# Kernel tuning notes

Hardware: AMD Instinct MI355X
Metric: run time of the kernel (lower is better)

## Reference

```python
import jax, jax.numpy as jnp
import numpy as np

D_MODEL = 1024
HEADS = 16
D_K = D_MODEL // HEADS  # 64


def setup_inputs() -> dict:
    key = jax.random.key(0)
    ks = jax.random.split(key, 9)
    B, S = 4, 2048
    values = jax.random.normal(ks[0], (B, S, D_MODEL), dtype=jnp.float32)
    keys = jax.random.normal(ks[1], (B, S, D_MODEL), dtype=jnp.float32)
    query = jax.random.normal(ks[2], (B, S, D_MODEL), dtype=jnp.float32)
    mask = jax.random.randint(ks[3], (1, 1, S, S), 0, 2, dtype=jnp.int32)
    # per-head projection weights (shared across heads), torch Linear layout (out, in)
    sc = 1.0 / np.sqrt(D_K)
    Wv = jax.random.uniform(ks[4], (D_K, D_K), jnp.float32, -sc, sc)
    Wk = jax.random.uniform(ks[5], (D_K, D_K), jnp.float32, -sc, sc)
    Wq = jax.random.uniform(ks[6], (D_K, D_K), jnp.float32, -sc, sc)
    so = 1.0 / np.sqrt(D_MODEL)
    Wo = jax.random.uniform(ks[7], (D_MODEL, D_MODEL), jnp.float32, -so, so)
    bo = jax.random.uniform(ks[8], (D_MODEL,), jnp.float32, -so, so)
    return {"values": values, "keys": keys, "query": query, "mask": mask,
            "Wv": Wv, "Wk": Wk, "Wq": Wq, "Wo": Wo, "bo": bo}


def reference(values, keys, query, mask, Wv, Wk, Wq, Wo, bo):
    n, q_len, d = query.shape
    v_len, k_len = values.shape[1], keys.shape[1]
    # reshape to (n, len, heads, d_k) and apply shared per-head linear (x @ W^T)
    v = values.reshape(n, v_len, HEADS, D_K) @ Wv.T
    k = keys.reshape(n, k_len, HEADS, D_K) @ Wk.T
    q = query.reshape(n, q_len, HEADS, D_K) @ Wq.T
    # scores: (n, h, q, k)
    scores = jnp.einsum('nqhd,nkhd->nhqk', q, k)
    scores = jnp.where(mask == 0, jnp.float32(-1e20), scores)
    attn = jax.nn.softmax(scores / jnp.sqrt(jnp.float32(D_K)), axis=3)
    out = jnp.einsum('nhqk,nkhd->nqhd', attn, v).reshape(n, q_len, HEADS * D_K)
    return out @ Wo.T + bo
```

## Files before the change

kernel.cpp:

```cpp
#include <hip/hip_runtime.h>

#define B 4
#define S 2048
#define H 16
#define DK 64
#define DM 1024
#define NTILES (S / 64)
#define QSCALE 0.18033688011112042f

typedef __attribute__((ext_vector_type(8))) short    short8v;
typedef __attribute__((ext_vector_type(4))) short    short4v;
typedef __attribute__((ext_vector_type(4))) float    float4v;
typedef __attribute__((ext_vector_type(4))) unsigned uint4v;

__device__ __forceinline__ unsigned short f2bf(float f) {
    unsigned u = __float_as_uint(f);
    u += 0x7fffu + ((u >> 16) & 1u);
    return (unsigned short)(u >> 16);
}
__device__ __forceinline__ float bf2f(unsigned short h) {
    return __uint_as_float(((unsigned)h) << 16);
}
__device__ __forceinline__ unsigned pk2_rtz(float lo, float hi) {
    return __builtin_amdgcn_perm(__float_as_uint(hi), __float_as_uint(lo), 0x07060302u);
}
__device__ __forceinline__ float fast_exp2(float x) {
#if __has_builtin(__builtin_amdgcn_exp2f)
    return __builtin_amdgcn_exp2f(x);
#else
    return __expf(x * 0.69314718055994531f);
#endif
}
__device__ __forceinline__ short8v cvt8(float4 a, float4 b) {
    short8v r;
    r[0] = (short)f2bf(a.x); r[1] = (short)f2bf(a.y);
    r[2] = (short)f2bf(a.z); r[3] = (short)f2bf(a.w);
    r[4] = (short)f2bf(b.x); r[5] = (short)f2bf(b.y);
    r[6] = (short)f2bf(b.z); r[7] = (short)f2bf(b.w);
    return r;
}
__device__ __forceinline__ void gl2lds16(const void* g, void* l) {
    __builtin_amdgcn_global_load_lds(
        (const __attribute__((address_space(1))) unsigned int*)g,
        (__attribute__((address_space(3))) unsigned int*)l, 16, 0, 0);
}

__global__ __launch_bounds__(256) void mask_pack_kernel(
    const int* __restrict__ mask, unsigned long long* __restrict__ mp)
{
    int t = blockIdx.x * 256 + threadIdx.x;
    int m = mask[t];
    unsigned long long b = __ballot(m != 0);
    if ((threadIdx.x & 63) == 0) mp[t >> 6] = b;
}

__global__ __launch_bounds__(256) void wsplit_kernel(
    const float* __restrict__ Wo, unsigned short* __restrict__ Wh,
    unsigned short* __restrict__ Wl)
{
    int t = (blockIdx.x * 256 + threadIdx.x) * 4;
    float4 wv = *(const float4*)(Wo + t);
    float ws4[4] = {wv.x, wv.y, wv.z, wv.w};
    short4v hv, lv;
    #pragma unroll
    for (int i = 0; i < 4; ++i) {
        unsigned short hi = f2bf(ws4[i]);
        hv[i] = (short)hi;
        lv[i] = (short)f2bf(ws4[i] - bf2f(hi));
    }
    *(short4v*)(Wh + t) = hv;
    *(short4v*)(Wl + t) = lv;
}

__global__ __launch_bounds__(256) void qkv_proj_kernel(
    const float* __restrict__ xv, const float* __restrict__ xk, const float* __restrict__ xq,
    const float* __restrict__ Wv, const float* __restrict__ Wk, const float* __restrict__ Wq,
    unsigned short* __restrict__ vtw, unsigned short* __restrict__ kw, unsigned short* __restrict__ qw)
{
    const int y = blockIdx.y;
    const float* x; const float* W;
    if (y == 0)      { x = xv; W = Wv; }
    else if (y == 1) { x = xk; W = Wk; }
    else             { x = xq; W = Wq; }

    const int tid = threadIdx.x;
    const int w = tid >> 6, L = tid & 63, a = L & 15, g = L >> 4;
    const int bx  = blockIdx.x;
    const int st  = bx & 31;
    const int bh  = bx >> 5;
    const int b_  = bh >> 4, h = bh & 15;
    const int s0b = st * 64;

    short8v wF[4][2];
    #pragma unroll
    for (int t = 0; t < 4; ++t)
        #pragma unroll
        for (int c = 0; c < 2; ++c) {
            const float* wr = W + (size_t)(16 * t + a) * 64 + 32 * c + 8 * g;
            wF[t][c] = cvt8(*(const float4*)wr, *(const float4*)(wr + 4));
        }

    const float* xr = x + ((size_t)(b_ * S) + s0b + 16 * w + a) * DM + h * 64 + 8 * g;
    short8v xF0 = cvt8(*(const float4*)(xr),      *(const float4*)(xr + 4));
    short8v xF1 = cvt8(*(const float4*)(xr + 32), *(const float4*)(xr + 36));

    const float4v z4 = {0.0f, 0.0f, 0.0f, 0.0f};

    if (y == 0) {
        const int c   = 16 * w + a;
        const int pos = 32 * (c >> 5) + 8 * ((c >> 2) & 3) + 4 * ((c >> 4) & 1) + (c & 3);
        #pragma unroll
        for (int mt = 0; mt < 4; ++mt) {
            float4v D = __builtin_amdgcn_mfma_f32_16x16x32_bf16(wF[mt][0], xF0, z4, 0, 0, 0);
            D = __builtin_amdgcn_mfma_f32_16x16x32_bf16(wF[mt][1], xF1, D, 0, 0, 0);
            #pragma unroll
            for (int r = 0; r < 4; ++r)
                vtw[((size_t)bh * 64 + 16 * mt + 4 * g + r) * S + s0b + pos] = f2bf(D[r]);
        }
    } else {
        unsigned short* out = (y == 1) ? kw : qw;
        const float scale = (y == 2) ? QSCALE : 1.0f;
        #pragma unroll
        for (int nt = 0; nt < 4; ++nt) {
            float4v D = __builtin_amdgcn_mfma_f32_16x16x32_bf16(xF0, wF[nt][0], z4, 0, 0, 0);
            D = __builtin_amdgcn_mfma_f32_16x16x32_bf16(xF1, wF[nt][1], D, 0, 0, 0);
            #pragma unroll
            for (int r = 0; r < 4; ++r)
                out[((size_t)bh * S + s0b + 16 * w + 4 * g + r) * 64 + 16 * nt + a] =
                    f2bf(D[r] * scale);
        }
    }
}

__global__ __launch_bounds__(256, 4) void flash_attn_kernel(
    const unsigned short* __restrict__ q, const unsigned short* __restrict__ k,
    const unsigned short* __restrict__ vt, const unsigned long long* __restrict__ mp,
    unsigned short* __restrict__ outh, unsigned short* __restrict__ outl)
{
    __shared__ unsigned short KV[2][2][64 * 64];

    const int tid = threadIdx.x;
    const int w   = tid >> 6;
    const int L   = tid & 63;
    const int a   = L & 15;
    const int g   = L >> 4;
    const int bh  = blockIdx.x;
    const int b_  = bh >> 4, h = bh & 15;
    const int qs  = blockIdx.y * 128 + w * 32;

    const unsigned short* qb = q  + (size_t)bh * S * 64;
    const unsigned short* kb = k  + (size_t)bh * S * 64;
    const unsigned short* vb = vt + (size_t)bh * 64 * S;

    short8v qB[2][2];
    #pragma unroll
    for (int gq = 0; gq < 2; ++gq) {
        const unsigned short* qr = qb + (size_t)(qs + 16 * gq + a) * 64;
        qB[gq][0] = *(const short8v*)(qr +      g * 8);
        qB[gq][1] = *(const short8v*)(qr + 32 + g * 8);
    }

    const unsigned long long* mr0 = mp + (size_t)(qs      + a) * NTILES;
    const unsigned long long* mr1 = mp + (size_t)(qs + 16 + a) * NTILES;

    int srow[2], schk[2];
    #pragma unroll
    for (int i = 0; i < 2; ++i) {
        int p   = (w * 2 + i) * 64 + L;
        srow[i] = p >> 3;
        schk[i] = (p & 7) ^ (srow[i] & 7);
    }

    short8v ones;
    #pragma unroll
    for (int i = 0; i < 8; ++i) ones[i] = (short)0x3F80;

    const float4v z4 = {0.0f, 0.0f, 0.0f, 0.0f};
    float4v o[2][4] = {{z4, z4, z4, z4}, {z4, z4, z4, z4}};
    float4v lD[2] = {z4, z4};

    #pragma unroll
    for (int i = 0; i < 2; ++i) {
        gl2lds16(kb + (size_t)srow[i] * 64 + schk[i] * 8, &KV[0][0][(w * 2 + i) * 64 * 8]);
        gl2lds16(vb + (size_t)srow[i] * S + schk[i] * 8,  &KV[0][1][(w * 2 + i) * 64 * 8]);
    }

    for (int kt = 0; kt < NTILES; ++kt) {
        const int cur = kt & 1;
        __syncthreads();

        if (kt + 1 < NTILES) {
            const int nk = kt + 1;
            #pragma unroll
            for (int i = 0; i < 2; ++i) {
                gl2lds16(kb + ((size_t)(nk * 64 + srow[i])) * 64 + schk[i] * 8,
                         &KV[cur ^ 1][0][(w * 2 + i) * 64 * 8]);
                gl2lds16(vb + (size_t)srow[i] * S + nk * 64 + schk[i] * 8,
                         &KV[cur ^ 1][1][(w * 2 + i) * 64 * 8]);
            }
        }

        const unsigned long long mw0 = mr0[kt];
        const unsigned long long mw1 = mr1[kt];

        const unsigned short* Kb = &KV[cur][0][0];
        const unsigned short* Vb = &KV[cur][1][0];

        short8v kB[4][2], vA[4][2];
        #pragma unroll
        for (int nt = 0; nt < 4; ++nt)
            #pragma unroll
            for (int c = 0; c < 2; ++c) {
                const int off = ((16 * nt + a) * 8 + ((4 * c + g) ^ (a & 7))) * 8;
                kB[nt][c] = *(const short8v*)(Kb + off);
                vA[nt][c] = *(const short8v*)(Vb + off);
            }

        #pragma unroll
        for (int gq = 0; gq < 2; ++gq) {
            float4v st[4];
            #pragma unroll
            for (int nt = 0; nt < 4; ++nt) {
                st[nt] = __builtin_amdgcn_mfma_f32_16x16x32_bf16(kB[nt][0], qB[gq][0], z4, 0, 0, 0);
                st[nt] = __builtin_amdgcn_mfma_f32_16x16x32_bf16(kB[nt][1], qB[gq][1], st[nt], 0, 0, 0);
            }

            const unsigned long long mw = gq ? mw1 : mw0;
            float e[4][4];
            #pragma unroll
            for (int nt = 0; nt < 4; ++nt) {
                unsigned bnt = (unsigned)(mw >> (16 * nt + 4 * g));
                #pragma unroll
                for (int r = 0; r < 4; ++r) {
                    float ee = fast_exp2(st[nt][r]);
                    e[nt][r] = ((bnt >> r) & 1u) ? ee : 0.0f;
                }
            }

            short8v pB[2];
            #pragma unroll
            for (int c = 0; c < 2; ++c) {
                uint4v pu;
                pu[0] = pk2_rtz(e[2*c  ][0], e[2*c  ][1]);
                pu[1] = pk2_rtz(e[2*c  ][2], e[2*c  ][3]);
                pu[2] = pk2_rtz(e[2*c+1][0], e[2*c+1][1]);
                pu[3] = pk2_rtz(e[2*c+1][2], e[2*c+1][3]);
                union { uint4v u; short8v s; } cvt;
                cvt.u = pu;
                pB[c] = cvt.s;
            }

            #pragma unroll
            for (int nt = 0; nt < 4; ++nt) {
                o[gq][nt] = __builtin_amdgcn_mfma_f32_16x16x32_bf16(vA[nt][0], pB[0], o[gq][nt], 0, 0, 0);
                o[gq][nt] = __builtin_amdgcn_mfma_f32_16x16x32_bf16(vA[nt][1], pB[1], o[gq][nt], 0, 0, 0);
            }
            lD[gq] = __builtin_amdgcn_mfma_f32_16x16x32_bf16(ones, pB[0], lD[gq], 0, 0, 0);
            lD[gq] = __builtin_amdgcn_mfma_f32_16x16x32_bf16(ones, pB[1], lD[gq], 0, 0, 0);
        }
    }

    #pragma unroll
    for (int gq = 0; gq < 2; ++gq) {
        const float inv = 1.0f / lD[gq][0];
        const size_t row = (size_t)(b_ * S + qs + 16 * gq + a);
        #pragma unroll
        for (int nt = 0; nt < 4; ++nt) {
            short4v hv, lv;
            #pragma unroll
            for (int r = 0; r < 4; ++r) {
                float v = o[gq][nt][r] * inv;
                unsigned short hi = f2bf(v);
                hv[r] = (short)hi;
                lv[r] = (short)f2bf(v - bf2f(hi));
            }
            const size_t off = row * DM + h * 64 + 16 * nt + 4 * g;
            *(short4v*)(outh + off) = hv;
            *(short4v*)(outl + off) = lv;
        }
    }
}

__global__ __launch_bounds__(256, 2) void out_proj_kernel(
    const unsigned short* __restrict__ Xh, const unsigned short* __restrict__ Xl,
    const unsigned short* __restrict__ Wh, const unsigned short* __restrict__ Wl,
    const float* __restrict__ bo, float* __restrict__ out)
{
    __shared__ unsigned short SAh[128 * 64], SAl[128 * 64];
    __shared__ unsigned short SBh[128 * 64], SBl[128 * 64];

    const int tid = threadIdx.x;
    const int w = tid >> 6, L = tid & 63, a = L & 15, g = L >> 4;
    const int wm = w >> 1, wn = w & 1;
    const int r0 = blockIdx.x * 128;
    const int n0 = blockIdx.y * 128;

    int prow[4], pchk[4], pbase[4];
    #pragma unroll
    for (int i = 0; i < 4; ++i) {
        int p    = w * 256 + i * 64 + L;
        prow[i]  = p >> 3;
        pchk[i]  = (p & 7) ^ (prow[i] & 7);
        pbase[i] = (w * 256 + i * 64) * 8;
    }

    const float4v z4 = {0.0f, 0.0f, 0.0f, 0.0f};
    float4v acc[4][4];
    #pragma unroll
    for (int mt = 0; mt < 4; ++mt)
        #pragma unroll
        for (int nt = 0; nt < 4; ++nt) acc[mt][nt] = z4;

    for (int kt = 0; kt < DM / 64; ++kt) {
        const int k0 = kt * 64;
        __syncthreads();
        #pragma unroll
        for (int i = 0; i < 4; ++i) {
            gl2lds16(Xh + (size_t)(r0 + prow[i]) * DM + k0 + pchk[i] * 8, &SAh[pbase[i]]);
            gl2lds16(Xl + (size_t)(r0 + prow[i]) * DM + k0 + pchk[i] * 8, &SAl[pbase[i]]);
            gl2lds16(Wh + (size_t)(n0 + prow[i]) * DM + k0 + pchk[i] * 8, &SBh[pbase[i]]);
            gl2lds16(Wl + (size_t)(n0 + prow[i]) * DM + k0 + pchk[i] * 8, &SBl[pbase[i]]);
        }
        __syncthreads();

        short8v bh_[4][2], bl_[4][2];
        #pragma unroll
        for (int nt = 0; nt < 4; ++nt)
            #pragma unroll
            for (int c = 0; c < 2; ++c) {
                const int rb  = 64 * wn + 16 * nt + a;
                const int off = (rb * 8 + ((4 * c + g) ^ (rb & 7))) * 8;
                bh_[nt][c] = *(const short8v*)&SBh[off];
                bl_[nt][c] = *(const short8v*)&SBl[off];
            }

        #pragma unroll
        for (int mt = 0; mt < 4; ++mt) {
            const int ra   = 64 * wm + 16 * mt + a;
            const int off0 = (ra * 8 + ((4 * 0 + g) ^ (ra & 7))) * 8;
            const int off1 = (ra * 8 + ((4 * 1 + g) ^ (ra & 7))) * 8;
            short8v ah0 = *(const short8v*)&SAh[off0];
            short8v ah1 = *(const short8v*)&SAh[off1];
            short8v al0 = *(const short8v*)&SAl[off0];
            short8v al1 = *(const short8v*)&SAl[off1];
            #pragma unroll
            for (int nt = 0; nt < 4; ++nt) {
                float4v acv = acc[mt][nt];
                acv = __builtin_amdgcn_mfma_f32_16x16x32_bf16(ah0, bh_[nt][0], acv, 0, 0, 0);
                acv = __builtin_amdgcn_mfma_f32_16x16x32_bf16(ah1, bh_[nt][1], acv, 0, 0, 0);
                acv = __builtin_amdgcn_mfma_f32_16x16x32_bf16(ah0, bl_[nt][0], acv, 0, 0, 0);
                acv = __builtin_amdgcn_mfma_f32_16x16x32_bf16(ah1, bl_[nt][1], acv, 0, 0, 0);
                acv = __builtin_amdgcn_mfma_f32_16x16x32_bf16(al0, bh_[nt][0], acv, 0, 0, 0);
                acv = __builtin_amdgcn_mfma_f32_16x16x32_bf16(al1, bh_[nt][1], acv, 0, 0, 0);
                acc[mt][nt] = acv;
            }
        }
    }

    #pragma unroll
    for (int mt = 0; mt < 4; ++mt) {
        const int m0 = r0 + 64 * wm + 16 * mt + 4 * g;
        #pragma unroll
        for (int nt = 0; nt < 4; ++nt) {
            const int n = n0 + 64 * wn + 16 * nt + a;
            const float bias = bo[n];
            #pragma unroll
            for (int r = 0; r < 4; ++r)
                out[(size_t)(m0 + r) * DM + n] = acc[mt][nt][r] + bias;
        }
    }
}

extern "C" void kernel_launch(void* const* d_in, const int* in_sizes, int n_in,
                              void* d_out, int out_size, void* d_ws, size_t ws_size,
                              hipStream_t stream) {
    (void)in_sizes; (void)n_in; (void)out_size; (void)ws_size;
    const float* values = (const float*)d_in[0];
    const float* keys   = (const float*)d_in[1];
    const float* query  = (const float*)d_in[2];
    const int*   mask   = (const int*)d_in[3];
    const float* Wv     = (const float*)d_in[4];
    const float* Wk     = (const float*)d_in[5];
    const float* Wq     = (const float*)d_in[6];
    const float* Wo     = (const float*)d_in[7];
    const float* bo     = (const float*)d_in[8];
    float* out = (float*)d_out;

    const size_t per = (size_t)B * H * S * DK;
    unsigned short* qw  = (unsigned short*)d_ws;
    unsigned short* kw  = qw + per;
    unsigned short* vtw = kw + per;
    unsigned long long* mp = (unsigned long long*)(vtw + per);
    unsigned short* atth = (unsigned short*)(mp + (size_t)S * S / 64);
    unsigned short* attl = atth + per;
    unsigned short* woh  = attl + per;
    unsigned short* wol  = woh + (size_t)DM * DM;

    mask_pack_kernel<<<S * S / 256, 256, 0, stream>>>(mask, mp);
    wsplit_kernel<<<DM * DM / 1024, 256, 0, stream>>>(Wo, woh, wol);

    dim3 g1(B * H * (S / 64), 3);
    qkv_proj_kernel<<<g1, 256, 0, stream>>>(values, keys, query, Wv, Wk, Wq, vtw, kw, qw);

    dim3 g2(B * H, S / 128);
    flash_attn_kernel<<<g2, 256, 0, stream>>>(qw, kw, vtw, mp, atth, attl);

    dim3 g3(B * S / 128, DM / 128);
    out_proj_kernel<<<g3, 256, 0, stream>>>(atth, attl, woh, wol, bo, out);
}
```

Measured before the change: 344.4 us.

## Switch to fp16 MFMA, drop split-bf16 out-projection, double-buffer out_proj loads

Moves all intermediates (Q, K, V^T, attention output, Wo) from bf16 to fp16 and uses fp16 MFMA instructions. The out-projection no longer uses a hi/lo bf16 split, so its MFMA count drops from six to two per tile and the attention kernel writes one output buffer instead of two. out_proj now double-buffers its global-to-LDS loads to overlap them with compute. The trade-off is fp16's narrower range: activations or weights that exceed it, or values that underflow it, could lose accuracy.

New measurement: 357.1 us. 1.04x slower.

```diff
diff --git a/kernel.cpp b/kernel.cpp
--- a/kernel.cpp
+++ b/kernel.cpp
@@ -8,21 +8,16 @@
 #define NTILES (S / 64)
 #define QSCALE 0.18033688011112042f
 
-typedef __attribute__((ext_vector_type(8))) short    short8v;
-typedef __attribute__((ext_vector_type(4))) short    short4v;
+typedef _Float16 half_t;
+typedef __attribute__((ext_vector_type(8))) _Float16 half8v;
+typedef __attribute__((ext_vector_type(2))) _Float16 half2v;
+typedef __attribute__((ext_vector_type(2))) __fp16   fp16x2;
 typedef __attribute__((ext_vector_type(4))) float    float4v;
-typedef __attribute__((ext_vector_type(4))) unsigned uint4v;
-
-__device__ __forceinline__ unsigned short f2bf(float f) {
-    unsigned u = __float_as_uint(f);
-    u += 0x7fffu + ((u >> 16) & 1u);
-    return (unsigned short)(u >> 16);
-}
-__device__ __forceinline__ float bf2f(unsigned short h) {
-    return __uint_as_float(((unsigned)h) << 16);
-}
-__device__ __forceinline__ unsigned pk2_rtz(float lo, float hi) {
-    return __builtin_amdgcn_perm(__float_as_uint(hi), __float_as_uint(lo), 0x07060302u);
+
+__device__ __forceinline__ unsigned pkh(float lo, float hi) {
+    union { fp16x2 h; unsigned u; } cvt;
+    cvt.h = __builtin_amdgcn_cvt_pkrtz(lo, hi);
+    return cvt.u;
 }
 __device__ __forceinline__ float fast_exp2(float x) {
 #if __has_builtin(__builtin_amdgcn_exp2f)
@@ -31,12 +26,10 @@
     return __expf(x * 0.69314718055994531f);
 #endif
 }
-__device__ __forceinline__ short8v cvt8(float4 a, float4 b) {
-    short8v r;
-    r[0] = (short)f2bf(a.x); r[1] = (short)f2bf(a.y);
-    r[2] = (short)f2bf(a.z); r[3] = (short)f2bf(a.w);
-    r[4] = (short)f2bf(b.x); r[5] = (short)f2bf(b.y);
-    r[6] = (short)f2bf(b.z); r[7] = (short)f2bf(b.w);
+__device__ __forceinline__ half8v cvt8h(float4 a, float4 b) {
+    half8v r;
+    r[0] = (half_t)a.x; r[1] = (half_t)a.y; r[2] = (half_t)a.z; r[3] = (half_t)a.w;
+    r[4] = (half_t)b.x; r[5] = (half_t)b.y; r[6] = (half_t)b.z; r[7] = (half_t)b.w;
     return r;
 }
 __device__ __forceinline__ void gl2lds16(const void* g, void* l) {
@@ -54,28 +47,21 @@
     if ((threadIdx.x & 63) == 0) mp[t >> 6] = b;
 }
 
-__global__ __launch_bounds__(256) void wsplit_kernel(
-    const float* __restrict__ Wo, unsigned short* __restrict__ Wh,
-    unsigned short* __restrict__ Wl)
+__global__ __launch_bounds__(256) void wcvt_kernel(
+    const float* __restrict__ Wo, half_t* __restrict__ Wh)
 {
     int t = (blockIdx.x * 256 + threadIdx.x) * 4;
     float4 wv = *(const float4*)(Wo + t);
-    float ws4[4] = {wv.x, wv.y, wv.z, wv.w};
-    short4v hv, lv;
-    #pragma unroll
-    for (int i = 0; i < 4; ++i) {
-        unsigned short hi = f2bf(ws4[i]);
-        hv[i] = (short)hi;
-        lv[i] = (short)f2bf(ws4[i] - bf2f(hi));
-    }
-    *(short4v*)(Wh + t) = hv;
-    *(short4v*)(Wl + t) = lv;
+    union { half_t h[4]; uint2 u; } cvt;
+    cvt.h[0] = (half_t)wv.x; cvt.h[1] = (half_t)wv.y;
+    cvt.h[2] = (half_t)wv.z; cvt.h[3] = (half_t)wv.w;
+    *(uint2*)(Wh + t) = cvt.u;
 }
 
 __global__ __launch_bounds__(256) void qkv_proj_kernel(
     const float* __restrict__ xv, const float* __restrict__ xk, const float* __restrict__ xq,
     const float* __restrict__ Wv, const float* __restrict__ Wk, const float* __restrict__ Wq,
-    unsigned short* __restrict__ vtw, unsigned short* __restrict__ kw, unsigned short* __restrict__ qw)
+    half_t* __restrict__ vtw, half_t* __restrict__ kw, half_t* __restrict__ qw)
 {
     const int y = blockIdx.y;
     const float* x; const float* W;
@@ -91,18 +77,18 @@
     const int b_  = bh >> 4, h = bh & 15;
     const int s0b = st * 64;
 
-    short8v wF[4][2];
+    half8v wF[4][2];
     #pragma unroll
     for (int t = 0; t < 4; ++t)
         #pragma unroll
         for (int c = 0; c < 2; ++c) {
             const float* wr = W + (size_t)(16 * t + a) * 64 + 32 * c + 8 * g;
-            wF[t][c] = cvt8(*(const float4*)wr, *(const float4*)(wr + 4));
+            wF[t][c] = cvt8h(*(const float4*)wr, *(const float4*)(wr + 4));
         }
 
     const float* xr = x + ((size_t)(b_ * S) + s0b + 16 * w + a) * DM + h * 64 + 8 * g;
-    short8v xF0 = cvt8(*(const float4*)(xr),      *(const float4*)(xr + 4));
-    short8v xF1 = cvt8(*(const float4*)(xr + 32), *(const float4*)(xr + 36));
+    half8v xF0 = cvt8h(*(const float4*)(xr),      *(const float4*)(xr + 4));
+    half8v xF1 = cvt8h(*(const float4*)(xr + 32), *(const float4*)(xr + 36));
 
     const float4v z4 = {0.0f, 0.0f, 0.0f, 0.0f};
 
@@ -111,33 +97,33 @@
         const int pos = 32 * (c >> 5) + 8 * ((c >> 2) & 3) + 4 * ((c >> 4) & 1) + (c & 3);
         #pragma unroll
         for (int mt = 0; mt < 4; ++mt) {
-            float4v D = __builtin_amdgcn_mfma_f32_16x16x32_bf16(wF[mt][0], xF0, z4, 0, 0, 0);
-            D = __builtin_amdgcn_mfma_f32_16x16x32_bf16(wF[mt][1], xF1, D, 0, 0, 0);
+            float4v D = __builtin_amdgcn_mfma_f32_16x16x32_f16(wF[mt][0], xF0, z4, 0, 0, 0);
+            D = __builtin_amdgcn_mfma_f32_16x16x32_f16(wF[mt][1], xF1, D, 0, 0, 0);
             #pragma unroll
             for (int r = 0; r < 4; ++r)
-                vtw[((size_t)bh * 64 + 16 * mt + 4 * g + r) * S + s0b + pos] = f2bf(D[r]);
+                vtw[((size_t)bh * 64 + 16 * mt + 4 * g + r) * S + s0b + pos] = (half_t)D[r];
         }
     } else {
-        unsigned short* out = (y == 1) ? kw : qw;
+        half_t* out = (y == 1) ? kw : qw;
         const float scale = (y == 2) ? QSCALE : 1.0f;
         #pragma unroll
         for (int nt = 0; nt < 4; ++nt) {
-            float4v D = __builtin_amdgcn_mfma_f32_16x16x32_bf16(xF0, wF[nt][0], z4, 0, 0, 0);
-            D = __builtin_amdgcn_mfma_f32_16x16x32_bf16(xF1, wF[nt][1], D, 0, 0, 0);
+            float4v D = __builtin_amdgcn_mfma_f32_16x16x32_f16(xF0, wF[nt][0], z4, 0, 0, 0);
+            D = __builtin_amdgcn_mfma_f32_16x16x32_f16(xF1, wF[nt][1], D, 0, 0, 0);
             #pragma unroll
             for (int r = 0; r < 4; ++r)
                 out[((size_t)bh * S + s0b + 16 * w + 4 * g + r) * 64 + 16 * nt + a] =
-                    f2bf(D[r] * scale);
+                    (half_t)(D[r] * scale);
         }
     }
 }
 
 __global__ __launch_bounds__(256, 4) void flash_attn_kernel(
-    const unsigned short* __restrict__ q, const unsigned short* __restrict__ k,
-    const unsigned short* __restrict__ vt, const unsigned long long* __restrict__ mp,
-    unsigned short* __restrict__ outh, unsigned short* __restrict__ outl)
-{
-    __shared__ unsigned short KV[2][2][64 * 64];
+    const half_t* __restrict__ q, const half_t* __restrict__ k,
+    const half_t* __restrict__ vt, const unsigned long long* __restrict__ mp,
+    half_t* __restrict__ att)
+{
+    __shared__ half_t KV[2][2][64 * 64];
 
     const int tid = threadIdx.x;
     const int w   = tid >> 6;
@@ -148,16 +134,16 @@
     const int b_  = bh >> 4, h = bh & 15;
     const int qs  = blockIdx.y * 128 + w * 32;
 
-    const unsigned short* qb = q  + (size_t)bh * S * 64;
-    const unsigned short* kb = k  + (size_t)bh * S * 64;
-    const unsigned short* vb = vt + (size_t)bh * 64 * S;
-
-    short8v qB[2][2];
+    const half_t* qb = q  + (size_t)bh * S * 64;
+    const half_t* kb = k  + (size_t)bh * S * 64;
+    const half_t* vb = vt + (size_t)bh * 64 * S;
+
+    half8v qB[2][2];
     #pragma unroll
     for (int gq = 0; gq < 2; ++gq) {
-        const unsigned short* qr = qb + (size_t)(qs + 16 * gq + a) * 64;
-        qB[gq][0] = *(const short8v*)(qr +      g * 8);
-        qB[gq][1] = *(const short8v*)(qr + 32 + g * 8);
+        const half_t* qr = qb + (size_t)(qs + 16 * gq + a) * 64;
+        qB[gq][0] = *(const half8v*)(qr +      g * 8);
+        qB[gq][1] = *(const half8v*)(qr + 32 + g * 8);
     }
 
     const unsigned long long* mr0 = mp + (size_t)(qs      + a) * NTILES;
@@ -171,9 +157,9 @@
         schk[i] = (p & 7) ^ (srow[i] & 7);
     }
 
-    short8v ones;
-    #pragma unroll
-    for (int i = 0; i < 8; ++i) ones[i] = (short)0x3F80;
+    half8v ones;
+    #pragma unroll
+    for (int i = 0; i < 8; ++i) ones[i] = (half_t)1.0f;
 
     const float4v z4 = {0.0f, 0.0f, 0.0f, 0.0f};
     float4v o[2][4] = {{z4, z4, z4, z4}, {z4, z4, z4, z4}};
@@ -203,17 +189,17 @@
         const unsigned long long mw0 = mr0[kt];
         const unsigned long long mw1 = mr1[kt];
 
-        const unsigned short* Kb = &KV[cur][0][0];
-        const unsigned short* Vb = &KV[cur][1][0];
-
-        short8v kB[4][2], vA[4][2];
+        const half_t* Kb = &KV[cur][0][0];
+        const half_t* Vb = &KV[cur][1][0];
+
+        half8v kB[4][2], vA[4][2];
         #pragma unroll
         for (int nt = 0; nt < 4; ++nt)
             #pragma unroll
             for (int c = 0; c < 2; ++c) {
                 const int off = ((16 * nt + a) * 8 + ((4 * c + g) ^ (a & 7))) * 8;
-                kB[nt][c] = *(const short8v*)(Kb + off);
-                vA[nt][c] = *(const short8v*)(Vb + off);
+                kB[nt][c] = *(const half8v*)(Kb + off);
+                vA[nt][c] = *(const half8v*)(Vb + off);
             }
 
         #pragma unroll
@@ -221,8 +207,8 @@
             float4v st[4];
             #pragma unroll
             for (int nt = 0; nt < 4; ++nt) {
-                st[nt] = __builtin_amdgcn_mfma_f32_16x16x32_bf16(kB[nt][0], qB[gq][0], z4, 0, 0, 0);
-                st[nt] = __builtin_amdgcn_mfma_f32_16x16x32_bf16(kB[nt][1], qB[gq][1], st[nt], 0, 0, 0);
+                st[nt] = __builtin_amdgcn_mfma_f32_16x16x32_f16(kB[nt][0], qB[gq][0], z4, 0, 0, 0);
+                st[nt] = __builtin_amdgcn_mfma_f32_16x16x32_f16(kB[nt][1], qB[gq][1], st[nt], 0, 0, 0);
             }
 
             const unsigned long long mw = gq ? mw1 : mw0;
@@ -237,26 +223,24 @@
                 }
             }
 
-            short8v pB[2];
+            half8v pB[2];
             #pragma unroll
             for (int c = 0; c < 2; ++c) {
-                uint4v pu;
-                pu[0] = pk2_rtz(e[2*c  ][0], e[2*c  ][1]);
-                pu[1] = pk2_rtz(e[2*c  ][2], e[2*c  ][3]);
-                pu[2] = pk2_rtz(e[2*c+1][0], e[2*c+1][1]);
-                pu[3] = pk2_rtz(e[2*c+1][2], e[2*c+1][3]);
-                union { uint4v u; short8v s; } cvt;
-                cvt.u = pu;
-                pB[c] = cvt.s;
+                union { unsigned u[4]; half8v hv; } cvt;
+                cvt.u[0] = pkh(e[2*c  ][0], e[2*c  ][1]);
+                cvt.u[1] = pkh(e[2*c  ][2], e[2*c  ][3]);
+                cvt.u[2] = pkh(e[2*c+1][0], e[2*c+1][1]);
+                cvt.u[3] = pkh(e[2*c+1][2], e[2*c+1][3]);
+                pB[c] = cvt.hv;
             }
 
             #pragma unroll
             for (int nt = 0; nt < 4; ++nt) {
-                o[gq][nt] = __builtin_amdgcn_mfma_f32_16x16x32_bf16(vA[nt][0], pB[0], o[gq][nt], 0, 0, 0);
-                o[gq][nt] = __builtin_amdgcn_mfma_f32_16x16x32_bf16(vA[nt][1], pB[1], o[gq][nt], 0, 0, 0);
-            }
-            lD[gq] = __builtin_amdgcn_mfma_f32_16x16x32_bf16(ones, pB[0], lD[gq], 0, 0, 0);
-            lD[gq] = __builtin_amdgcn_mfma_f32_16x16x32_bf16(ones, pB[1], lD[gq], 0, 0, 0);
+                o[gq][nt] = __builtin_amdgcn_mfma_f32_16x16x32_f16(vA[nt][0], pB[0], o[gq][nt], 0, 0, 0);
+                o[gq][nt] = __builtin_amdgcn_mfma_f32_16x16x32_f16(vA[nt][1], pB[1], o[gq][nt], 0, 0, 0);
+            }
+            lD[gq] = __builtin_amdgcn_mfma_f32_16x16x32_f16(ones, pB[0], lD[gq], 0, 0, 0);
+            lD[gq] = __builtin_amdgcn_mfma_f32_16x16x32_f16(ones, pB[1], lD[gq], 0, 0, 0);
         }
     }
 
@@ -266,28 +250,19 @@
         const size_t row = (size_t)(b_ * S + qs + 16 * gq + a);
         #pragma unroll
         for (int nt = 0; nt < 4; ++nt) {
-            short4v hv, lv;
-            #pragma unroll
-            for (int r = 0; r < 4; ++r) {
-                float v = o[gq][nt][r] * inv;
-                unsigned short hi = f2bf(v);
-                hv[r] = (short)hi;
-                lv[r] = (short)f2bf(v - bf2f(hi));
-            }
-            const size_t off = row * DM + h * 64 + 16 * nt + 4 * g;
-            *(short4v*)(outh + off) = hv;
-            *(short4v*)(outl + off) = lv;
+            union { unsigned u[2]; uint2 u2; } cvt;
+            cvt.u[0] = pkh(o[gq][nt][0] * inv, o[gq][nt][1] * inv);
+            cvt.u[1] = pkh(o[gq][nt][2] * inv, o[gq][nt][3] * inv);
+            *(uint2*)(att + row * DM + h * 64 + 16 * nt + 4 * g) = cvt.u2;
         }
     }
 }
 
 __global__ __launch_bounds__(256, 2) void out_proj_kernel(
-    const unsigned short* __restrict__ Xh, const unsigned short* __restrict__ Xl,
-    const unsigned short* __restrict__ Wh, const unsigned short* __restrict__ Wl,
+    const half_t* __restrict__ X, const half_t* __restrict__ Wh,
     const float* __restrict__ bo, float* __restrict__ out)
 {
-    __shared__ unsigned short SAh[128 * 64], SAl[128 * 64];
-    __shared__ unsigned short SBh[128 * 64], SBl[128 * 64];
+    __shared__ half_t SA[2][128 * 64], SB[2][128 * 64];
 
     const int tid = threadIdx.x;
     const int w = tid >> 6, L = tid & 63, a = L & 15, g = L >> 4;
@@ -311,47 +286,47 @@
         #pragma unroll
         for (int nt = 0; nt < 4; ++nt) acc[mt][nt] = z4;
 
+    #pragma unroll
+    for (int i = 0; i < 4; ++i) {
+        gl2lds16(X  + (size_t)(r0 + prow[i]) * DM + pchk[i] * 8, &SA[0][pbase[i]]);
+        gl2lds16(Wh + (size_t)(n0 + prow[i]) * DM + pchk[i] * 8, &SB[0][pbase[i]]);
+    }
+
     for (int kt = 0; kt < DM / 64; ++kt) {
-        const int k0 = kt * 64;
+        const int cur = kt & 1;
         __syncthreads();
-        #pragma unroll
-        for (int i = 0; i < 4; ++i) {
-            gl2lds16(Xh + (size_t)(r0 + prow[i]) * DM + k0 + pchk[i] * 8, &SAh[pbase[i]]);
-            gl2lds16(Xl + (size_t)(r0 + prow[i]) * DM + k0 + pchk[i] * 8, &SAl[pbase[i]]);
-            gl2lds16(Wh + (size_t)(n0 + prow[i]) * DM + k0 + pchk[i] * 8, &SBh[pbase[i]]);
-            gl2lds16(Wl + (size_t)(n0 + prow[i]) * DM + k0 + pchk[i] * 8, &SBl[pbase[i]]);
-        }
-        __syncthreads();
-
-        short8v bh_[4][2], bl_[4][2];
+
+        if (kt + 1 < DM / 64) {
+            const int k0 = (kt + 1) * 64;
+            #pragma unroll
+            for (int i = 0; i < 4; ++i) {
+                gl2lds16(X  + (size_t)(r0 + prow[i]) * DM + k0 + pchk[i] * 8, &SA[cur ^ 1][pbase[i]]);
+                gl2lds16(Wh + (size_t)(n0 + prow[i]) * DM + k0 + pchk[i] * 8, &SB[cur ^ 1][pbase[i]]);
+            }
+        }
+
+        half8v bF[4][2];
         #pragma unroll
         for (int nt = 0; nt < 4; ++nt)
             #pragma unroll
             for (int c = 0; c < 2; ++c) {
                 const int rb  = 64 * wn + 16 * nt + a;
                 const int off = (rb * 8 + ((4 * c + g) ^ (rb & 7))) * 8;
-                bh_[nt][c] = *(const short8v*)&SBh[off];
-                bl_[nt][c] = *(const short8v*)&SBl[off];
+                bF[nt][c] = *(const half8v*)&SB[cur][off];
             }
 
         #pragma unroll
         for (int mt = 0; mt < 4; ++mt) {
             const int ra   = 64 * wm + 16 * mt + a;
-            const int off0 = (ra * 8 + ((4 * 0 + g) ^ (ra & 7))) * 8;
-            const int off1 = (ra * 8 + ((4 * 1 + g) ^ (ra & 7))) * 8;
-            short8v ah0 = *(const short8v*)&SAh[off0];
-            short8v ah1 = *(const short8v*)&SAh[off1];
-            short8v al0 = *(const short8v*)&SAl[off0];
-            short8v al1 = *(const short8v*)&SAl[off1];
+            const int off0 = (ra * 8 + ((0 + g) ^ (ra & 7))) * 8;
+            const int off1 = (ra * 8 + ((4 + g) ^ (ra & 7))) * 8;
+            half8v a0 = *(const half8v*)&SA[cur][off0];
+            half8v a1 = *(const half8v*)&SA[cur][off1];
             #pragma unroll
             for (int nt = 0; nt < 4; ++nt) {
                 float4v acv = acc[mt][nt];
-                acv = __builtin_amdgcn_mfma_f32_16x16x32_bf16(ah0, bh_[nt][0], acv, 0, 0, 0);
-                acv = __builtin_amdgcn_mfma_f32_16x16x32_bf16(ah1, bh_[nt][1], acv, 0, 0, 0);
-                acv = __builtin_amdgcn_mfma_f32_16x16x32_bf16(ah0, bl_[nt][0], acv, 0, 0, 0);
-                acv = __builtin_amdgcn_mfma_f32_16x16x32_bf16(ah1, bl_[nt][1], acv, 0, 0, 0);
-                acv = __builtin_amdgcn_mfma_f32_16x16x32_bf16(al0, bh_[nt][0], acv, 0, 0, 0);
-                acv = __builtin_amdgcn_mfma_f32_16x16x32_bf16(al1, bh_[nt][1], acv, 0, 0, 0);
+                acv = __builtin_amdgcn_mfma_f32_16x16x32_f16(a0, bF[nt][0], acv, 0, 0, 0);
+                acv = __builtin_amdgcn_mfma_f32_16x16x32_f16(a1, bF[nt][1], acv, 0, 0, 0);
                 acc[mt][nt] = acv;
             }
         }
@@ -387,24 +362,22 @@
     float* out = (float*)d_out;
 
     const size_t per = (size_t)B * H * S * DK;
-    unsigned short* qw  = (unsigned short*)d_ws;
-    unsigned short* kw  = qw + per;
-    unsigned short* vtw = kw + per;
+    half_t* qw  = (half_t*)d_ws;
+    half_t* kw  = qw + per;
+    half_t* vtw = kw + per;
     unsigned long long* mp = (unsigned long long*)(vtw + per);
-    unsigned short* atth = (unsigned short*)(mp + (size_t)S * S / 64);
-    unsigned short* attl = atth + per;
-    unsigned short* woh  = attl + per;
-    unsigned short* wol  = woh + (size_t)DM * DM;
+    half_t* atth = (half_t*)(mp + (size_t)S * S / 64);
+    half_t* woh  = atth + per;
 
     mask_pack_kernel<<<S * S / 256, 256, 0, stream>>>(mask, mp);
-    wsplit_kernel<<<DM * DM / 1024, 256, 0, stream>>>(Wo, woh, wol);
+    wcvt_kernel<<<DM * DM / 1024, 256, 0, stream>>>(Wo, woh);
 
     dim3 g1(B * H * (S / 64), 3);
     qkv_proj_kernel<<<g1, 256, 0, stream>>>(values, keys, query, Wv, Wk, Wq, vtw, kw, qw);
 
     dim3 g2(B * H, S / 128);
-    flash_attn_kernel<<<g2, 256, 0, stream>>>(qw, kw, vtw, mp, atth, attl);
+    flash_attn_kernel<<<g2, 256, 0, stream>>>(qw, kw, vtw, mp, atth);
 
     dim3 g3(B * S / 128, DM / 128);
-    out_proj_kernel<<<g3, 256, 0, stream>>>(atth, attl, woh, wol, bo, out);
-}
+    out_proj_kernel<<<g3, 256, 0, stream>>>(atth, woh, bo, out);
+}
```
